# Performance work log

Hardware: AMD Instinct MI355X
Metric: run time of the kernel (lower is better)

The kernel has to match this reference:

```python
import jax, jax.numpy as jnp
import numpy as np

B, T, C, H = 4, 1024, 768, 12
HD = C // H  # 64
EPS = 1e-5

def setup_inputs() -> dict:
    key = jax.random.key(0)
    ks = jax.random.split(key, 6)
    s = 0.02
    return {
        "x": jax.random.normal(ks[0], (B, T, C), jnp.float32),
        "ln1_w": jnp.ones((C,), jnp.float32),
        "w_attn": jax.random.normal(ks[1], (C, 3 * C), jnp.float32) * s,
        "w_pos": jax.random.normal(ks[2], (C, C), jnp.float32) * s,
        "w_cproj": jax.random.normal(ks[3], (C, C), jnp.float32) * s,
        "ln2_w": jnp.ones((C,), jnp.float32),
        "w_fc": jax.random.normal(ks[4], (C, 4 * C), jnp.float32) * s,
        "w_mproj": jax.random.normal(ks[5], (4 * C, C), jnp.float32) * s,
    }

def _layernorm(x, w):
    m = jnp.mean(x, axis=-1, keepdims=True)
    v = jnp.mean(jnp.square(x - m), axis=-1, keepdims=True)
    return (x - m) * jax.lax.rsqrt(v + EPS) * w

def _rpe_table(dtype):
    # sinusoidal table over relative distances [-(T-1), T-1] -> [2T-1, HD]
    inv_freq = 1.0 / (10000.0 ** (jnp.arange(0, HD, 2, dtype=jnp.float32) / HD))
    dist = jnp.arange(-(T - 1), T, dtype=jnp.float32)
    freqs = dist[:, None] * inv_freq[None, :]
    return jnp.concatenate([jnp.sin(freqs), jnp.cos(freqs)], axis=-1).astype(dtype)

def reference(x, ln1_w, w_attn, w_pos, w_cproj, ln2_w, w_fc, w_mproj):
    # ---- attention branch ----
    h = _layernorm(x, ln1_w)
    qkv = h @ w_attn                                 # [B,T,3C]
    q, k, v = jnp.split(qkv, 3, axis=-1)
    q = q.reshape(B, T, H, HD).transpose(0, 2, 1, 3)  # [B,H,T,HD]
    k = k.reshape(B, T, H, HD).transpose(0, 2, 1, 3)
    v = v.reshape(B, T, H, HD).transpose(0, 2, 1, 3)
    # note: the original also computes p = c_pos(x) but never uses it (dead code)

    # relative position embeddings gathered to [T,T,HD]
    idx = jnp.arange(T)
    rel = jnp.clip(idx[:, None] - idx[None, :], -(T - 1), T - 1) + (T - 1)
    rpe = _rpe_table(q.dtype)[rel]                    # [T,T,HD]

    scale = 1.0 / np.sqrt(HD)
    att = (jnp.einsum('bhid,bhjd->bhij', q, k)
           + jnp.einsum('bhid,ijd->bhij', q, rpe)) * scale
    causal = idx[:, None] >= idx[None, :]             # [T,T] lower-tri
    att = jnp.where(causal, att, -jnp.inf)
    att = jax.nn.softmax(att, axis=-1)
    y = jnp.einsum('bhij,bhjd->bhid', att, v)         # [B,H,T,HD]
    y = y.transpose(0, 2, 1, 3).reshape(B, T, C) @ w_cproj
    x = x + y

    # ---- MLP branch ----
    h2 = _layernorm(x, ln2_w)
    m = jax.nn.gelu(h2 @ w_fc, approximate=False) @ w_mproj
    return x + m
```

## Files before the change

kernel.cpp:

```cpp
#include <hip/hip_runtime.h>
#include <math.h>

typedef __attribute__((ext_vector_type(8))) short bf16x8;
typedef __attribute__((ext_vector_type(4))) float f32x4;
typedef __attribute__((ext_vector_type(16))) float f32x16;
typedef __attribute__((ext_vector_type(4))) unsigned u32x4;

__device__ inline short f2bf(float f) {
  unsigned u = __builtin_bit_cast(unsigned, f);
  u = u + 0x7fffu + ((u >> 16) & 1u);
  return (short)(u >> 16);
}
__device__ inline float bf2f(short s) {
  return __builtin_bit_cast(float, ((unsigned)(unsigned short)s) << 16);
}
__device__ inline unsigned cvt_pk_bf16(float lo, float hi) {
  unsigned r;
  asm("v_cvt_pk_bf16_f32 %0, %1, %2" : "=v"(r) : "v"(lo), "v"(hi));
  return r;
}

__device__ inline void gload16(const short* g, const short* l) {
  __builtin_amdgcn_global_load_lds(
      (const __attribute__((address_space(1))) unsigned*)g,
      (__attribute__((address_space(3))) unsigned*)(short*)l, 16, 0, 0);
}

__global__ __launch_bounds__(256) void wtrans_all(
    const float* __restrict__ wa, const float* __restrict__ wc,
    const float* __restrict__ wf, const float* __restrict__ wm,
    short* __restrict__ oa, short* __restrict__ oc,
    short* __restrict__ of, short* __restrict__ om,
    const float* __restrict__ x, const float* __restrict__ ln1_w,
    short* __restrict__ h_bf) {
  __shared__ float tile[32][33];
  int blk = blockIdx.x;
  const int tid = threadIdx.x;
  if (blk >= 6912) {
    const int row = blk - 6912;
    const float* xr = x + (size_t)row * 768;
    float v0 = xr[tid], v1 = xr[tid + 256], v2 = xr[tid + 512];
    float s = v0 + v1 + v2;
    #pragma unroll
    for (int o = 1; o < 64; o <<= 1) s += __shfl_xor(s, o);
    __shared__ float red[8];
    const int wv = tid >> 6;
    if ((tid & 63) == 0) red[wv] = s;
    __syncthreads();
    const float mean = (red[0] + red[1] + red[2] + red[3]) * (1.0f / 768.0f);
    v0 -= mean; v1 -= mean; v2 -= mean;
    float q = v0 * v0 + v1 * v1 + v2 * v2;
    #pragma unroll
    for (int o = 1; o < 64; o <<= 1) q += __shfl_xor(q, o);
    if ((tid & 63) == 0) red[4 + wv] = q;
    __syncthreads();
    const float var = (red[4] + red[5] + red[6] + red[7]) * (1.0f / 768.0f);
    const float inv = 1.0f / sqrtf(var + 1e-5f);
    h_bf[(size_t)row * 768 + tid]       = f2bf(v0 * inv * ln1_w[tid]);
    h_bf[(size_t)row * 768 + tid + 256] = f2bf(v1 * inv * ln1_w[tid + 256]);
    h_bf[(size_t)row * 768 + tid + 512] = f2bf(v2 * inv * ln1_w[tid + 512]);
    return;
  }
  const float* in; short* out; int K, N, bx;
  if (blk < 1728)      { in = wa; out = oa; K = 768;  N = 2304; bx = 72; }
  else if (blk < 2304) { blk -= 1728; in = wc; out = oc; K = 768;  N = 768;  bx = 24; }
  else if (blk < 4608) { blk -= 2304; in = wf; out = of; K = 768;  N = 3072; bx = 96; }
  else                 { blk -= 4608; in = wm; out = om; K = 3072; N = 768;  bx = 24; }
  const int n0 = (blk % bx) * 32, k0 = (blk / bx) * 32;
  const int tx = tid & 31, ty = tid >> 5;
  #pragma unroll
  for (int r = ty; r < 32; r += 8)
    tile[r][tx] = in[(size_t)(k0 + r) * N + n0 + tx];
  __syncthreads();
  #pragma unroll
  for (int r = ty; r < 32; r += 8)
    out[(size_t)(n0 + r) * K + k0 + tx] = f2bf(tile[tx][r]);
}

__global__ __launch_bounds__(256) void qv_kernel(
    const short* __restrict__ qkv, short* __restrict__ qpr,
    short* __restrict__ ktab, short* __restrict__ vT) {
  __shared__ short tile[64][65];
  if (blockIdx.x < 768) {
    const int idx = blockIdx.x * 256 + threadIdx.x;
    const int row = idx >> 2;
    const int cc0 = (idx & 3) * 8;
    const int i = row & 1023, bh = row >> 10;
    const int b = bh / 12, h = bh % 12;
    const short* q = qkv + (size_t)(b * 1024 + i) * 2304 + h * 64;
    const bf16x8 q8s = *(const bf16x8*)(q + cc0);
    const bf16x8 q8c = *(const bf16x8*)(q + 32 + cc0);
    bf16x8 o1, o2, kc, ks;
    #pragma unroll
    for (int j = 0; j < 8; ++j) {
      const int cc = cc0 + j;
      const float invf = exp2f(-(float)cc * (13.287712379549449f / 32.0f));
      const float ang = (float)i * invf;
      float si, co;
      __sincosf(ang, &si, &co);
      const float qs = bf2f(q8s[j]), qc = bf2f(q8c[j]);
      o1[j] = f2bf(qs * si + qc * co);
      o2[j] = f2bf(qc * si - qs * co);
      kc[j] = f2bf(co);
      ks[j] = f2bf(si);
    }
    *(bf16x8*)(qpr + (size_t)row * 64 + cc0)      = o1;
    *(bf16x8*)(qpr + (size_t)row * 64 + 32 + cc0) = o2;
    if (bh == 0) {
      *(bf16x8*)(ktab + i * 64 + cc0)      = kc;
      *(bf16x8*)(ktab + i * 64 + 32 + cc0) = ks;
    }
  } else {
    const int blk = blockIdx.x - 768;
    const int bh = blk >> 4, t0 = (blk & 15) * 64;
    const int b = bh / 12, h = bh % 12;
    const int tx = threadIdx.x & 63, ty = threadIdx.x >> 6;
    const short* src = qkv + (size_t)(b * 1024 + t0) * 2304 + 1536 + h * 64;
    #pragma unroll
    for (int r = ty; r < 64; r += 4)
      tile[r][tx] = src[(size_t)r * 2304 + tx];
    __syncthreads();
    short* dst = vT + (size_t)bh * 64 * 1024 + t0;
    #pragma unroll
    for (int r = ty; r < 64; r += 4)
      dst[(size_t)r * 1024 + tx] = tile[tx][r];
  }
}

__global__ __launch_bounds__(256) void ln_kernel(
    const float* __restrict__ x, const float* __restrict__ w,
    short* __restrict__ out) {
  const int row = blockIdx.x, tid = threadIdx.x;
  const float* xr = x + (size_t)row * 768;
  float v0 = xr[tid], v1 = xr[tid + 256], v2 = xr[tid + 512];
  float s = v0 + v1 + v2;
  #pragma unroll
  for (int o = 1; o < 64; o <<= 1) s += __shfl_xor(s, o);
  __shared__ float red[8];
  const int wv = tid >> 6;
  if ((tid & 63) == 0) red[wv] = s;
  __syncthreads();
  const float mean = (red[0] + red[1] + red[2] + red[3]) * (1.0f / 768.0f);
  v0 -= mean; v1 -= mean; v2 -= mean;
  float q = v0 * v0 + v1 * v1 + v2 * v2;
  #pragma unroll
  for (int o = 1; o < 64; o <<= 1) q += __shfl_xor(q, o);
  if ((tid & 63) == 0) red[4 + wv] = q;
  __syncthreads();
  const float var = (red[4] + red[5] + red[6] + red[7]) * (1.0f / 768.0f);
  const float inv = 1.0f / sqrtf(var + 1e-5f);
  out[(size_t)row * 768 + tid]       = f2bf(v0 * inv * w[tid]);
  out[(size_t)row * 768 + tid + 256] = f2bf(v1 * inv * w[tid + 256]);
  out[(size_t)row * 768 + tid + 512] = f2bf(v2 * inv * w[tid + 512]);
}

template <int EPI, int BM, int BN>
__global__ __launch_bounds__(256) void gemm3u(
    const short* __restrict__ A, const short* __restrict__ Bt,
    const float* __restrict__ res, float* __restrict__ outF,
    short* __restrict__ outB, int M, int N, int K, int lda, int ldb) {
  __shared__ __align__(16) short As[3][BM * 32];
  __shared__ __align__(16) short Bs[3][BN * 32];
  constexpr int WM = BM / 2, WN = BN / 2;
  constexpr int MI = WM / 16, NJ = WN / 16;
  constexpr int NA = BM / 64, NB = BN / 64;
  constexpr int G = NA + NB;
  const int tid = threadIdx.x;
  const int w = tid >> 6, lane = tid & 63;
  const int gx = gridDim.x, gy = gridDim.y;
  const int nwg = gx * gy * gridDim.z;
  const int lin = blockIdx.x + gx * (blockIdx.y + gy * blockIdx.z);
  const int wg = (lin & 7) * (nwg >> 3) + (lin >> 3);
  const int bxi = wg % gx;
  const int tmp = wg / gx;
  const int byi = tmp % gy, bzi = tmp / gy;
  const int m0 = byi * BM, n0 = bxi * BN;
  const int wm = (w >> 1) * WM, wn = (w & 1) * WN;
  const int lr = lane >> 2;
  const int lc = (((lane & 3) ^ ((lr >> 1) & 3))) * 8;
  if constexpr (EPI == 3) {
    A += (size_t)bzi * K;
    Bt += (size_t)bzi * K;
    outF += (size_t)bzi * (size_t)M * N;
  }
  f32x4 acc[MI][NJ];
  #pragma unroll
  for (int i = 0; i < MI; i++)
    #pragma unroll
    for (int j = 0; j < NJ; j++)
      #pragma unroll
      for (int r = 0; r < 4; r++) acc[i][j][r] = 0.0f;

  const int nt = K / 32;
  const short* pA[NA];
  const short* pB[NB];
  #pragma unroll
  for (int p = 0; p < NA; ++p)
    pA[p] = A + (size_t)(m0 + p * 64 + w * 16 + lr) * lda + lc;
  #pragma unroll
  for (int p = 0; p < NB; ++p)
    pB[p] = Bt + (size_t)(n0 + p * 64 + w * 16 + lr) * ldb + lc;
  const int fr = lane & 15, c4 = lane >> 4;
  const int aoff = (wm + fr) * 32 + ((c4 ^ ((fr >> 1) & 3))) * 8;
  const int boff = (wn + fr) * 32 + ((c4 ^ ((fr >> 1) & 3))) * 8;

#define STAGE(SB)                                                              \
  do {                                                                         \
    _Pragma("unroll") for (int p = 0; p < NA; ++p) {                           \
      gload16(pA[p], &As[SB][p * 2048 + w * 512]);                             \
      pA[p] += 32;                                                             \
    }                                                                          \
    _Pragma("unroll") for (int p = 0; p < NB; ++p) {                           \
      gload16(pB[p], &Bs[SB][p * 2048 + w * 512]);                             \
      pB[p] += 32;                                                             \
    }                                                                          \
  } while (0)

#define STEP(CB, SB, DOSTAGE, LAST)                                            \
  do {                                                                         \
    if (LAST) asm volatile("s_waitcnt vmcnt(0)" ::: "memory");                 \
    else      asm volatile("s_waitcnt vmcnt(%0)" :: "n"(G) : "memory");        \
    __builtin_amdgcn_s_barrier();                                              \
    __builtin_amdgcn_sched_barrier(0);                                         \
    bf16x8 af[MI], bfr[NJ];                                                    \
    _Pragma("unroll") for (int i = 0; i < MI; i++)                             \
      af[i] = *(const bf16x8*)&As[CB][aoff + i * 512];                         \
    _Pragma("unroll") for (int j = 0; j < NJ; j++)                             \
      bfr[j] = *(const bf16x8*)&Bs[CB][boff + j * 512];                        \
    if (DOSTAGE) STAGE(SB);                                                    \
    _Pragma("unroll") for (int i = 0; i < MI; i++)                             \
      _Pragma("unroll") for (int j = 0; j < NJ; j++)                           \
        acc[i][j] = __builtin_amdgcn_mfma_f32_16x16x32_bf16(                   \
            af[i], bfr[j], acc[i][j], 0, 0, 0);                                \
  } while (0)

  STAGE(0);
  STAGE(1);
  const int ntri = nt / 3;
  for (int ti = 0; ti < ntri - 1; ++ti) {
    STEP(0, 2, 1, 0);
    STEP(1, 0, 1, 0);
    STEP(2, 1, 1, 0);
  }
  STEP(0, 2, 1, 0);
  STEP(1, 0, 0, 0);
  STEP(2, 0, 0, 1);
#undef STEP
#undef STAGE

  const int r0 = (lane >> 4) * 4, cl = lane & 15;
  #pragma unroll
  for (int i = 0; i < MI; i++) {
    #pragma unroll
    for (int j = 0; j < NJ; j++) {
      const int gm = m0 + wm + i * 16 + r0;
      const int gn = n0 + wn + j * 16 + cl;
      #pragma unroll
      for (int r = 0; r < 4; r++) {
        const size_t idx = (size_t)(gm + r) * N + gn;
        const float v = acc[i][j][r];
        if constexpr (EPI == 0) {
          outB[idx] = f2bf(v);
        } else if constexpr (EPI == 1) {
          outF[idx] = res[idx] + v;
        } else if constexpr (EPI == 2) {
          outB[idx] = f2bf(0.5f * v * (1.0f + erff(v * 0.70710678118f)));
        } else {
          outF[idx] = v;
        }
      }
    }
  }
}

__global__ __launch_bounds__(256) void reduce_splitk(
    const float* __restrict__ Cp, const float* __restrict__ res,
    float* __restrict__ out) {
  const size_t i4 = ((size_t)blockIdx.x * 256 + threadIdx.x) * 4;
  float4 a = *(const float4*)(res + i4);
  #pragma unroll
  for (int z = 0; z < 2; ++z) {
    float4 p = *(const float4*)(Cp + (size_t)z * 3145728 + i4);
    a.x += p.x; a.y += p.y; a.z += p.z; a.w += p.w;
  }
  *(float4*)(out + i4) = a;
}

__global__ __launch_bounds__(512) void attn_part8(
    const short* __restrict__ qkv, const short* __restrict__ vT,
    const short* __restrict__ qpr, const short* __restrict__ ktab,
    float* __restrict__ mpart, float* __restrict__ lpart,
    short* __restrict__ Ypart) {
  __shared__ __align__(16) short Ka[2][32 * 136];
  __shared__ __align__(16) short Va[2][64 * 40];
  const int bx = blockIdx.x;
  const int bh = bx / 20;
  const int r = bx % 20;
  int c, sub;
  if (r < 4)        { c = 0; sub = r; }
  else if (r < 8)   { c = 1; sub = r - 4; }
  else if (r < 11)  { c = 2; sub = r - 8; }
  else if (r < 14)  { c = 3; sub = r - 11; }
  else if (r < 16)  { c = 4; sub = r - 14; }
  else if (r < 18)  { c = 5; sub = r - 16; }
  else if (r == 18) { c = 6; sub = 0; }
  else              { c = 7; sub = 0; }
  const int tid = threadIdx.x;
  const int w = tid >> 6;
  const int lane = tid & 63;
  const int li = lane & 31, hi = lane >> 5;
  const int it = 4 * c + sub * 8 + w;
  const bool valid = (it <= 31);
  const int b = bh / 12, h = bh % 12;
  const int I0 = (valid ? it : 31) * 32;
  const int jt0 = 4 * c;
  const int jtmax = valid ? ((it < jt0 + 3) ? it : jt0 + 3) : (jt0 - 1);
  constexpr float SCALE2 = 0.125f * 1.44269504089f;

  const short* kbase = qkv + (size_t)(b * 1024) * 2304 + 768 + h * 64;
  const short* vbase = vT + (size_t)bh * 64 * 1024;

  const int krow = tid >> 4, kch = tid & 15;
  const short* ksrc = (kch < 8) ? (kbase + kch * 8) : (ktab + (kch - 8) * 8);
  const size_t kstr = (kch < 8) ? 2304 : 64;
  const int vrow = tid >> 2, vch = tid & 3;

  int4 kreg, vreg;
  {
    const int J0 = jt0 * 32;
    kreg = *(const int4*)(ksrc + (size_t)(J0 + krow) * kstr);
    if (tid < 256)
      vreg = *(const int4*)(vbase + (size_t)vrow * 1024 + J0 + vch * 8);
  }

  const short* qrow = qkv + (size_t)(b * 1024 + I0 + li) * 2304 + h * 64;
  const short* qprow = qpr + ((size_t)bh * 1024 + I0 + li) * 64;
  bf16x8 qf[8];
  #pragma unroll
  for (int s = 0; s < 4; s++) {
    qf[s]     = *(const bf16x8*)(qrow + s * 16 + hi * 8);
    qf[4 + s] = *(const bf16x8*)(qprow + s * 16 + hi * 8);
  }

  *(int4*)&Ka[0][krow * 136 + kch * 8] = kreg;
  if (tid < 256) *(int4*)&Va[0][vrow * 40 + vch * 8] = vreg;
  __syncthreads();

  float m_run = -1e30f, l_run = 0.0f;
  f32x16 ya0, ya1;
  #pragma unroll
  for (int q = 0; q < 16; q++) { ya0[q] = 0.0f; ya1[q] = 0.0f; }

  for (int t = 0; t < 4; ++t) {
    const int cur = t & 1;
    if (t < 3) {
      const int J0n = (jt0 + t + 1) * 32;
      kreg = *(const int4*)(ksrc + (size_t)(J0n + krow) * kstr);
      if (tid < 256)
        vreg = *(const int4*)(vbase + (size_t)vrow * 1024 + J0n + vch * 8);
    }
    const int jt = jt0 + t;
    if (jt <= jtmax) {
      bf16x8 kf[8];
      #pragma unroll
      for (int s = 0; s < 8; s++)
        kf[s] = *(const bf16x8*)&Ka[cur][li * 136 + s * 16 + hi * 8];
      bf16x8 vc[4];
      #pragma unroll
      for (int s = 0; s < 2; s++) {
        vc[s * 2]     = *(const bf16x8*)&Va[cur][li * 40 + s * 16 + hi * 8];
        vc[s * 2 + 1] = *(const bf16x8*)&Va[cur][(32 + li) * 40 + s * 16 + hi * 8];
      }
      f32x16 sa0, sa1;
      #pragma unroll
      for (int q = 0; q < 16; q++) { sa0[q] = 0.0f; sa1[q] = 0.0f; }
      __builtin_amdgcn_s_setprio(1);
      #pragma unroll
      for (int s = 0; s < 4; s++) {
        sa0 = __builtin_amdgcn_mfma_f32_32x32x16_bf16(kf[2 * s],     qf[2 * s],     sa0, 0, 0, 0);
        sa1 = __builtin_amdgcn_mfma_f32_32x32x16_bf16(kf[2 * s + 1], qf[2 * s + 1], sa1, 0, 0, 0);
      }
      __builtin_amdgcn_s_setprio(0);
      float sv[16];
      float mx = -1e30f;
      if (jt == it) {
        #pragma unroll
        for (int q = 0; q < 16; q++) {
          const int j = (q & 3) + 8 * (q >> 2) + 4 * hi;
          float v = (sa0[q] + sa1[q]) * SCALE2;
          v = (j <= li) ? v : -1e30f;
          sv[q] = v;
          mx = fmaxf(mx, v);
        }
      } else {
        #pragma unroll
        for (int q = 0; q < 16; q++) {
          const float v = (sa0[q] + sa1[q]) * SCALE2;
          sv[q] = v;
          mx = fmaxf(mx, v);
        }
      }
      mx = fmaxf(mx, __shfl_xor(mx, 32));
      float mref = m_run;
      float alpha = 1.0f;
      const bool resc = !__all(mx <= m_run + 11.5f);
      if (resc) {
        mref = fmaxf(m_run, mx);
        alpha = exp2f(m_run - mref);
        m_run = mref;
      }
      float psum = 0.0f;
      unsigned pw[8];
      #pragma unroll
      for (int q = 0; q < 8; q++) {
        const float p0 = exp2f(sv[2 * q] - mref);
        const float p1 = exp2f(sv[2 * q + 1] - mref);
        psum += p0 + p1;
        pw[q] = cvt_pk_bf16(p0, p1);
      }
      psum += __shfl_xor(psum, 32);
      l_run = l_run * alpha + psum;
      if (resc) {
        #pragma unroll
        for (int q = 0; q < 16; q++) {
          const int row = (q & 3) + 8 * (q >> 2) + 4 * hi;
          const float a = __shfl(alpha, row);
          ya0[q] *= a;
          ya1[q] *= a;
        }
      }
      #pragma unroll
      for (int s = 0; s < 2; s++) {
        unsigned a0 = pw[4 * s],     b0 = pw[4 * s + 2];
        unsigned a1 = pw[4 * s + 1], b1 = pw[4 * s + 3];
        asm volatile("v_permlane32_swap_b32 %0, %1" : "+v"(a0), "+v"(b0));
        asm volatile("v_permlane32_swap_b32 %0, %1" : "+v"(a1), "+v"(b1));
        u32x4 t4;
        t4[0] = a0; t4[1] = a1; t4[2] = b0; t4[3] = b1;
        const bf16x8 pf = __builtin_bit_cast(bf16x8, t4);
        __builtin_amdgcn_s_setprio(1);
        ya0 = __builtin_amdgcn_mfma_f32_32x32x16_bf16(pf, vc[s * 2],     ya0, 0, 0, 0);
        ya1 = __builtin_amdgcn_mfma_f32_32x32x16_bf16(pf, vc[s * 2 + 1], ya1, 0, 0, 0);
        __builtin_amdgcn_s_setprio(0);
      }
    }
    if (t < 3) {
      *(int4*)&Ka[cur ^ 1][krow * 136 + kch * 8] = kreg;
      if (tid < 256) *(int4*)&Va[cur ^ 1][vrow * 40 + vch * 8] = vreg;
    }
    __syncthreads();
  }
  if (!valid) return;
  const int task = bh * 144 + it + 30 * c - 2 * c * c;
  if (hi == 0) {
    mpart[(size_t)task * 32 + li] = m_run;
    lpart[(size_t)task * 32 + li] = l_run;
  }
  short* yb = Ypart + (size_t)task * 2048;
  #pragma unroll
  for (int q = 0; q < 16; q++) {
    const int row = (q & 3) + 8 * (q >> 2) + 4 * hi;
    yb[row * 64 + li]      = f2bf(ya0[q]);
    yb[row * 64 + 32 + li] = f2bf(ya1[q]);
  }
}

__global__ __launch_bounds__(256) void attn_combine(
    const float* __restrict__ mpart, const float* __restrict__ lpart,
    const short* __restrict__ Ypart, short* __restrict__ yout) {
  const int blk = blockIdx.x;
  const int it = blk & 31, bh = blk >> 5;
  const int b = bh / 12, h = bh % 12;
  const int g = it >> 2;
  const int nc = g + 1;
  const int row = threadIdx.x >> 3;
  const int c0 = (threadIdx.x & 7) * 8;
  float mv[8], lv[8], wgt[8];
  float m = -1e30f;
  #pragma unroll
  for (int cI = 0; cI < 8; ++cI) {
    const int idx = bh * 144 + it + 30 * cI - 2 * cI * cI;
    mv[cI] = (cI < nc) ? mpart[(size_t)idx * 32 + row] : -1e30f;
    lv[cI] = (cI < nc) ? lpart[(size_t)idx * 32 + row] : 0.0f;
    m = fmaxf(m, mv[cI]);
  }
  float L = 0.0f;
  #pragma unroll
  for (int cI = 0; cI < 8; ++cI) {
    wgt[cI] = exp2f(mv[cI] - m);
    L += lv[cI] * wgt[cI];
  }
  const float inv = 1.0f / L;
  float y[8];
  #pragma unroll
  for (int r = 0; r < 8; r++) y[r] = 0.0f;
  #pragma unroll
  for (int cI = 0; cI < 8; ++cI) {
    if (cI < nc) {
      const int idx = bh * 144 + it + 30 * cI - 2 * cI * cI;
      bf16x8 v = *(const bf16x8*)(Ypart + ((size_t)idx * 32 + row) * 64 + c0);
      #pragma unroll
      for (int r = 0; r < 8; r++) y[r] += bf2f(v[r]) * wgt[cI];
    }
  }
  short* dst = yout + (size_t)(b * 1024 + it * 32 + row) * 768 + h * 64 + c0;
  #pragma unroll
  for (int r = 0; r < 8; r++) dst[r] = f2bf(y[r] * inv);
}

extern "C" void kernel_launch(void* const* d_in, const int* in_sizes, int n_in,
                              void* d_out, int out_size, void* d_ws, size_t ws_size,
                              hipStream_t stream) {
  const float* x       = (const float*)d_in[0];
  const float* ln1_w   = (const float*)d_in[1];
  const float* w_attn  = (const float*)d_in[2];
  const float* w_cproj = (const float*)d_in[4];
  const float* ln2_w   = (const float*)d_in[5];
  const float* w_fc    = (const float*)d_in[6];
  const float* w_mproj = (const float*)d_in[7];
  float* out = (float*)d_out;
  char* ws = (char*)d_ws;

  short* wT_attn  = (short*)(ws + 0);
  short* wT_cproj = (short*)(ws + 3538944);
  short* wT_fc    = (short*)(ws + 4718592);
  short* wT_mproj = (short*)(ws + 9437184);
  short* ktab     = (short*)(ws + 14155776);
  short* h_bf     = (short*)(ws + 14417920);
  short* qpr      = (short*)(ws + 14417920);
  short* qkv_bf   = (short*)(ws + 20709376);
  short* vT       = (short*)(ws + 39583744);
  short* y_att    = (short*)(ws + 45875200);
  short* h2_bf    = (short*)(ws + 52166656);
  short* hfc_bf   = (short*)(ws + 58458112);
  float* mpart = (float*)(ws + 52166656);
  float* lpart = (float*)(ws + 53051392);
  short* Ypart = (short*)(ws + 53936128);
  float* Cpart = (float*)(ws + 20709376);

  wtrans_all<<<11008, 256, 0, stream>>>(w_attn, w_cproj, w_fc, w_mproj,
                                        wT_attn, wT_cproj, wT_fc, wT_mproj,
                                        x, ln1_w, h_bf);

  gemm3u<0, 128, 128><<<dim3(18, 32), 256, 0, stream>>>(
      h_bf, wT_attn, nullptr, nullptr, qkv_bf, 4096, 2304, 768, 768, 768);
  qv_kernel<<<1536, 256, 0, stream>>>(qkv_bf, qpr, ktab, vT);
  attn_part8<<<960, 512, 0, stream>>>(qkv_bf, vT, qpr, ktab, mpart, lpart, Ypart);
  attn_combine<<<1536, 256, 0, stream>>>(mpart, lpart, Ypart, y_att);
  gemm3u<1, 64, 64><<<dim3(12, 64), 256, 0, stream>>>(
      y_att, wT_cproj, x, out, nullptr, 4096, 768, 768, 768, 768);
  ln_kernel<<<4096, 256, 0, stream>>>(out, ln2_w, h2_bf);
  gemm3u<2, 128, 128><<<dim3(24, 32), 256, 0, stream>>>(
      h2_bf, wT_fc, nullptr, nullptr, hfc_bf, 4096, 3072, 768, 768, 768);
  gemm3u<3, 128, 64><<<dim3(12, 32, 2), 256, 0, stream>>>(
      hfc_bf, wT_mproj, nullptr, Cpart, nullptr, 4096, 768, 1536, 3072, 3072);
  reduce_splitk<<<3072, 256, 0, stream>>>(Cpart, out, out);
}
```

Baseline: 188.6 us.

## Fuse V transpose into QKV GEMM epilogue and pack weight-transpose stores

```diff
diff --git a/kernel.cpp b/kernel.cpp
--- a/kernel.cpp
+++ b/kernel.cpp
@@ -72,58 +72,45 @@
   for (int r = ty; r < 32; r += 8)
     tile[r][tx] = in[(size_t)(k0 + r) * N + n0 + tx];
   __syncthreads();
-  #pragma unroll
-  for (int r = ty; r < 32; r += 8)
-    out[(size_t)(n0 + r) * K + k0 + tx] = f2bf(tile[tx][r]);
+  const int kx = tid & 15, ny = tid >> 4;
+  #pragma unroll
+  for (int r = ny; r < 32; r += 16) {
+    const unsigned lo = (unsigned)(unsigned short)f2bf(tile[2 * kx][r]);
+    const unsigned hi = (unsigned)(unsigned short)f2bf(tile[2 * kx + 1][r]);
+    *(unsigned*)&out[(size_t)(n0 + r) * K + k0 + 2 * kx] = lo | (hi << 16);
+  }
 }
 
 __global__ __launch_bounds__(256) void qv_kernel(
     const short* __restrict__ qkv, short* __restrict__ qpr,
-    short* __restrict__ ktab, short* __restrict__ vT) {
-  __shared__ short tile[64][65];
-  if (blockIdx.x < 768) {
-    const int idx = blockIdx.x * 256 + threadIdx.x;
-    const int row = idx >> 2;
-    const int cc0 = (idx & 3) * 8;
-    const int i = row & 1023, bh = row >> 10;
-    const int b = bh / 12, h = bh % 12;
-    const short* q = qkv + (size_t)(b * 1024 + i) * 2304 + h * 64;
-    const bf16x8 q8s = *(const bf16x8*)(q + cc0);
-    const bf16x8 q8c = *(const bf16x8*)(q + 32 + cc0);
-    bf16x8 o1, o2, kc, ks;
-    #pragma unroll
-    for (int j = 0; j < 8; ++j) {
-      const int cc = cc0 + j;
-      const float invf = exp2f(-(float)cc * (13.287712379549449f / 32.0f));
-      const float ang = (float)i * invf;
-      float si, co;
-      __sincosf(ang, &si, &co);
-      const float qs = bf2f(q8s[j]), qc = bf2f(q8c[j]);
-      o1[j] = f2bf(qs * si + qc * co);
-      o2[j] = f2bf(qc * si - qs * co);
-      kc[j] = f2bf(co);
-      ks[j] = f2bf(si);
-    }
-    *(bf16x8*)(qpr + (size_t)row * 64 + cc0)      = o1;
-    *(bf16x8*)(qpr + (size_t)row * 64 + 32 + cc0) = o2;
-    if (bh == 0) {
-      *(bf16x8*)(ktab + i * 64 + cc0)      = kc;
-      *(bf16x8*)(ktab + i * 64 + 32 + cc0) = ks;
-    }
-  } else {
-    const int blk = blockIdx.x - 768;
-    const int bh = blk >> 4, t0 = (blk & 15) * 64;
-    const int b = bh / 12, h = bh % 12;
-    const int tx = threadIdx.x & 63, ty = threadIdx.x >> 6;
-    const short* src = qkv + (size_t)(b * 1024 + t0) * 2304 + 1536 + h * 64;
-    #pragma unroll
-    for (int r = ty; r < 64; r += 4)
-      tile[r][tx] = src[(size_t)r * 2304 + tx];
-    __syncthreads();
-    short* dst = vT + (size_t)bh * 64 * 1024 + t0;
-    #pragma unroll
-    for (int r = ty; r < 64; r += 4)
-      dst[(size_t)r * 1024 + tx] = tile[tx][r];
+    short* __restrict__ ktab) {
+  const int idx = blockIdx.x * 256 + threadIdx.x;
+  const int row = idx >> 2;
+  const int cc0 = (idx & 3) * 8;
+  const int i = row & 1023, bh = row >> 10;
+  const int b = bh / 12, h = bh % 12;
+  const short* q = qkv + (size_t)(b * 1024 + i) * 2304 + h * 64;
+  const bf16x8 q8s = *(const bf16x8*)(q + cc0);
+  const bf16x8 q8c = *(const bf16x8*)(q + 32 + cc0);
+  bf16x8 o1, o2, kc, ks;
+  #pragma unroll
+  for (int j = 0; j < 8; ++j) {
+    const int cc = cc0 + j;
+    const float invf = exp2f(-(float)cc * (13.287712379549449f / 32.0f));
+    const float ang = (float)i * invf;
+    float si, co;
+    __sincosf(ang, &si, &co);
+    const float qs = bf2f(q8s[j]), qc = bf2f(q8c[j]);
+    o1[j] = f2bf(qs * si + qc * co);
+    o2[j] = f2bf(qc * si - qs * co);
+    kc[j] = f2bf(co);
+    ks[j] = f2bf(si);
+  }
+  *(bf16x8*)(qpr + (size_t)row * 64 + cc0)      = o1;
+  *(bf16x8*)(qpr + (size_t)row * 64 + 32 + cc0) = o2;
+  if (bh == 0) {
+    *(bf16x8*)(ktab + i * 64 + cc0)      = kc;
+    *(bf16x8*)(ktab + i * 64 + 32 + cc0) = ks;
   }
 }
 
@@ -265,8 +252,19 @@
           outF[idx] = res[idx] + v;
         } else if constexpr (EPI == 2) {
           outB[idx] = f2bf(0.5f * v * (1.0f + erff(v * 0.70710678118f)));
+        } else if constexpr (EPI == 3) {
+          outF[idx] = v;
         } else {
-          outF[idx] = v;
+          if (gn < 1536) {
+            outB[idx] = f2bf(v);
+          } else {
+            short* vTp = (short*)outF;
+            const int gmr = gm + r;
+            const int bq = gmr >> 10, t = gmr & 1023;
+            const int hd = gn - 1536;
+            vTp[((size_t)((bq * 12 + (hd >> 6)) * 64 + (hd & 63))) * 1024 + t] =
+                f2bf(v);
+          }
         }
       }
     }
@@ -542,9 +540,9 @@
                                         wT_attn, wT_cproj, wT_fc, wT_mproj,
                                         x, ln1_w, h_bf);
 
-  gemm3u<0, 128, 128><<<dim3(18, 32), 256, 0, stream>>>(
-      h_bf, wT_attn, nullptr, nullptr, qkv_bf, 4096, 2304, 768, 768, 768);
-  qv_kernel<<<1536, 256, 0, stream>>>(qkv_bf, qpr, ktab, vT);
+  gemm3u<4, 128, 128><<<dim3(18, 32), 256, 0, stream>>>(
+      h_bf, wT_attn, nullptr, (float*)vT, qkv_bf, 4096, 2304, 768, 768, 768);
+  qv_kernel<<<768, 256, 0, stream>>>(qkv_bf, qpr, ktab);
   attn_part8<<<960, 512, 0, stream>>>(qkv_bf, vT, qpr, ktab, mpart, lpart, Ypart);
   attn_combine<<<1536, 256, 0, stream>>>(mpart, lpart, Ypart, y_att);
   gemm3u<1, 64, 64><<<dim3(12, 64), 256, 0, stream>>>(
```

Result: slower. 199.5 us, median of 2 (+5.7%).
